# Kernel optimization log

Measured on AMD Instinct MI355X. Metric: run time of the kernel, lower is better.

The kernel has to match this reference:

```python
import jax, jax.numpy as jnp
import numpy as np

INPUT_DIM = 1024
LATENT_DIM = 100
NUM_EMBEDDINGS = 21
COMMITMENT_COST = 0.1
BATCH = 65536


def setup_inputs() -> dict:
    key = jax.random.key(0)
    k_x, k_we, k_be, k_cb, k_wd, k_bd = jax.random.split(key, 6)
    x = jax.random.normal(k_x, (BATCH, INPUT_DIM), dtype=jnp.float32)
    # nn.Linear default init ~ U(-1/sqrt(fan_in), 1/sqrt(fan_in)); approx with scaled uniform
    s_e = 1.0 / np.sqrt(INPUT_DIM)
    W_enc = jax.random.uniform(k_we, (LATENT_DIM, INPUT_DIM), jnp.float32, -s_e, s_e)
    b_enc = jax.random.uniform(k_be, (LATENT_DIM,), jnp.float32, -s_e, s_e)
    # codebook init ~ U(-1/num_embeddings, 1/num_embeddings)
    s_c = 1.0 / NUM_EMBEDDINGS
    codebook = jax.random.uniform(k_cb, (NUM_EMBEDDINGS, LATENT_DIM), jnp.float32, -s_c, s_c)
    s_d = 1.0 / np.sqrt(LATENT_DIM)
    W_dec = jax.random.uniform(k_wd, (INPUT_DIM, LATENT_DIM), jnp.float32, -s_d, s_d)
    b_dec = jax.random.uniform(k_bd, (INPUT_DIM,), jnp.float32, -s_d, s_d)
    return {"x": x, "W_enc": W_enc, "b_enc": b_enc, "codebook": codebook,
            "W_dec": W_dec, "b_dec": b_dec}


def reference(x, W_enc, b_enc, codebook, W_dec, b_dec):
    # Encoder: (B, D_in) -> (B, L)
    z_e = x @ W_enc.T + b_enc
    # Squared L2 distances to codebook: (B, K)
    distances = (jnp.sum(z_e ** 2, axis=-1, keepdims=True)
                 + jnp.sum(codebook ** 2, axis=1)[None, :]
                 - 2.0 * (z_e @ codebook.T))
    encoding_indices = jnp.argmin(distances, axis=-1, keepdims=True)  # (B, 1) int
    z_q = codebook[encoding_indices[:, 0]]  # (B, L)
    sg = jax.lax.stop_gradient
    vq_loss = (jnp.mean((sg(z_q) - z_e) ** 2)
               + COMMITMENT_COST * jnp.mean((sg(z_e) - z_q) ** 2))
    # Straight-through estimator
    z_q_st = z_e + sg(z_q - z_e)
    # Decoder: (B, L) -> (B, D_in)
    x_recon = z_q_st @ W_dec.T + b_dec
    return (x_recon, vq_loss, encoding_indices)
```

## Files before the change

kernel.cpp:

```cpp
#include <hip/hip_runtime.h>
#include <hip/hip_bf16.h>

#define BATCH   65536
#define D       1024
#define L       100
#define C       21
#define NPAD    112

typedef __bf16 bf16x8 __attribute__((ext_vector_type(8)));
typedef float  f32x4  __attribute__((ext_vector_type(4)));

static constexpr size_t OFF_P  = 8192;
static constexpr size_t OFF_U  = OFF_P + (size_t)BATCH * 4;
static constexpr size_t OFF_T  = OFF_U + (size_t)C * D * 4;
static constexpr size_t OFF_R  = OFF_T + 128;
static constexpr size_t OFF_WB = OFF_R + (size_t)C * D * 4;

__global__ __launch_bounds__(256) void k_setup(
    const float* __restrict__ W_enc, const float* __restrict__ b_enc,
    const float* __restrict__ cb,    const float* __restrict__ W_dec,
    const float* __restrict__ b_dec,
    float* __restrict__ u, float* __restrict__ t, float* __restrict__ R,
    __bf16* __restrict__ Wb)
{
    int id = blockIdx.x * 256 + threadIdx.x;
    if (id < C * D) {
        int c = id >> 10, k = id & 1023;
        float s = 0.f;
        for (int j = 0; j < L; j++) s += cb[c * L + j] * W_enc[j * D + k];
        u[id] = s;
    } else if (id < 2 * C * D) {
        int i2 = id - C * D;
        int c = i2 >> 10, k = i2 & 1023;
        float s = 0.f;
        for (int j = 0; j < L; j++) s += cb[c * L + j] * W_dec[k * L + j];
        R[i2] = s + b_dec[k];
    } else if (id < 2 * C * D + NPAD * D) {
        int i3 = id - 2 * C * D;
        int n = i3 >> 10, k = i3 & 1023;
        Wb[i3] = (n < L) ? (__bf16)W_enc[n * D + k] : (__bf16)0.f;
    } else if (id < 2 * C * D + NPAD * D + C) {
        int c = id - 2 * C * D - NPAD * D;
        float s = 0.f, b2 = 0.f;
        for (int j = 0; j < L; j++) {
            float cv = cb[c * L + j];
            s  += cv * cv;
            b2 += b_enc[j] * cv;
        }
        t[c] = s - 2.f * b2;
    }
}

__global__ __launch_bounds__(256) void k_main(
    const float* __restrict__ x, const float* __restrict__ u,
    const float* __restrict__ t, const float* __restrict__ R,
    const __bf16* __restrict__ Wb, const float* __restrict__ b_enc,
    float* __restrict__ outR, float* __restrict__ outIdx,
    double* __restrict__ bsums)
{
    __shared__ float part[4][64][22];
    __shared__ float pbest[64];
    __shared__ int   idxs[64];
    __shared__ float bpart[16];

    const int lane = threadIdx.x & 63;
    const int wave = __builtin_amdgcn_readfirstlane(threadIdx.x >> 6);
    const int row0 = blockIdx.x * 64;
    const int n15  = lane & 15;
    const int q    = lane >> 4;

    float sacc[C];
#pragma unroll
    for (int c = 0; c < C; c++) sacc[c] = 0.f;
    f32x4 zacc[7];
#pragma unroll
    for (int nt = 0; nt < 7; nt++) zacc[nt] = (f32x4){0.f, 0.f, 0.f, 0.f};

    const float* xs = x + (size_t)(row0 + lane) * D + wave * 16;
    const float* ub = u + wave * 16;
    const float* xm = x + (size_t)(row0 + wave * 16 + n15) * D + q * 8;

    for (int k0 = 0; k0 < D; k0 += 64) {
#pragma unroll
        for (int j2 = 0; j2 < 4; j2++) {
            float4 xv = *(const float4*)(xs + k0 + j2 * 4);
#pragma unroll
            for (int c = 0; c < C; c++) {
                const float* uc = ub + c * D + k0 + j2 * 4;
                sacc[c] += xv.x * uc[0] + xv.y * uc[1] + xv.z * uc[2] + xv.w * uc[3];
            }
        }
#pragma unroll
        for (int ks = 0; ks < 2; ks++) {
            float4 a0 = *(const float4*)(xm + k0 + ks * 32);
            float4 a1 = *(const float4*)(xm + k0 + ks * 32 + 4);
            bf16x8 af;
            af[0] = (__bf16)a0.x; af[1] = (__bf16)a0.y; af[2] = (__bf16)a0.z; af[3] = (__bf16)a0.w;
            af[4] = (__bf16)a1.x; af[5] = (__bf16)a1.y; af[6] = (__bf16)a1.z; af[7] = (__bf16)a1.w;
#pragma unroll
            for (int nt = 0; nt < 7; nt++) {
                bf16x8 bfr = *(const bf16x8*)(Wb + (size_t)(nt * 16 + n15) * D + k0 + ks * 32 + q * 8);
                zacc[nt] = __builtin_amdgcn_mfma_f32_16x16x32_bf16(af, bfr, zacc[nt], 0, 0, 0);
            }
        }
        __builtin_amdgcn_s_barrier();
    }

#pragma unroll
    for (int c = 0; c < C; c++) part[wave][lane][c] = sacc[c];
    __syncthreads();
    if (wave == 0) {
        float best = 3.0e38f;
        int   bi   = 0;
#pragma unroll
        for (int c = 0; c < C; c++) {
            float s = part[0][lane][c] + part[1][lane][c]
                    + part[2][lane][c] + part[3][lane][c];
            float score = t[c] - 2.0f * s;
            if (score < best) { best = score; bi = c; }
        }
        idxs[lane]         = bi;
        pbest[lane]        = best;
        outIdx[row0 + lane] = (float)bi;
    }
    __syncthreads();

    float rn[4] = {0.f, 0.f, 0.f, 0.f};
#pragma unroll
    for (int nt = 0; nt < 7; nt++) {
        int col = nt * 16 + n15;
        float bn = (col < L) ? b_enc[col] : 0.f;
#pragma unroll
        for (int r = 0; r < 4; r++) {
            float z = zacc[nt][r] + bn;
            rn[r] += z * z;
        }
    }
#pragma unroll
    for (int off = 1; off < 16; off <<= 1) {
#pragma unroll
        for (int r = 0; r < 4; r++) rn[r] += __shfl_xor(rn[r], off, 64);
    }
    if (n15 == 0) {
        float s4 = 0.f;
#pragma unroll
        for (int r = 0; r < 4; r++) s4 += rn[r] + pbest[wave * 16 + q * 4 + r];
        bpart[wave * 4 + q] = s4;
    }
    __syncthreads();
    if (threadIdx.x == 0) {
        double bs = 0.0;
        for (int i = 0; i < 16; i++) bs += (double)bpart[i];
        bsums[blockIdx.x] = bs;
    }

    for (int r = 0; r < 64; r++) {
        int id = idxs[r];
        const f32x4 v = ((const f32x4*)(R + (size_t)id * D))[threadIdx.x];
        __builtin_nontemporal_store(v, ((f32x4*)(outR + (size_t)(row0 + r) * D)) + threadIdx.x);
    }
}

__global__ __launch_bounds__(256) void k_final(
    const double* __restrict__ bsums, float* __restrict__ out_loss)
{
    __shared__ double wsum[4];
    int t = threadIdx.x;
    double s = bsums[t] + bsums[t + 256] + bsums[t + 512] + bsums[t + 768];
    for (int off = 32; off; off >>= 1) s += __shfl_down(s, off, 64);
    if ((t & 63) == 0) wsum[t >> 6] = s;
    __syncthreads();
    if (t == 0) {
        double tot = wsum[0] + wsum[1] + wsum[2] + wsum[3];
        out_loss[0] = (float)(1.1 * tot / ((double)BATCH * (double)L));
    }
}

extern "C" void kernel_launch(void* const* d_in, const int* in_sizes, int n_in,
                              void* d_out, int out_size, void* d_ws, size_t ws_size,
                              hipStream_t stream) {
    const float* x     = (const float*)d_in[0];
    const float* W_enc = (const float*)d_in[1];
    const float* b_enc = (const float*)d_in[2];
    const float* cb    = (const float*)d_in[3];
    const float* W_dec = (const float*)d_in[4];
    const float* b_dec = (const float*)d_in[5];

    char*   ws    = (char*)d_ws;
    double* bsums = (double*)ws;
    float*  u     = (float*)(ws + OFF_U);
    float*  t     = (float*)(ws + OFF_T);
    float*  R     = (float*)(ws + OFF_R);
    __bf16* Wb    = (__bf16*)(ws + OFF_WB);

    float* outR    = (float*)d_out;
    float* outLoss = outR + (size_t)BATCH * D;
    float* outIdx  = outLoss + 1;

    k_setup<<<617, 256, 0, stream>>>(W_enc, b_enc, cb, W_dec, b_dec, u, t, R, Wb);
    k_main <<<BATCH / 64, 256, 0, stream>>>(x, u, t, R, Wb, b_enc, outR, outIdx, bsums);
    k_final<<<1, 256, 0, stream>>>(bsums, outLoss);
}
```

Baseline: 564.4 us.

## Stage x tiles through double-buffered LDS with register prefetch in main kernel

Each 64-column chunk of x is now loaded once per block with coalesced row-contiguous loads, prefetched into registers one chunk ahead, and stored into a double-buffered shared-memory tile. The scalar distance path and the MFMA A-operand both read from that tile instead of each issuing strided global loads of the same x data. The partial-sum scratch reuses the tile's storage, and launch bounds now request four blocks per CU. The aim is to remove duplicated, poorly coalesced global reads of x and to hide load latency. The cost is about 35KB of LDS per block, extra barriers, and more register pressure from the prefetch buffers.

```diff
diff --git a/kernel.cpp b/kernel.cpp
--- a/kernel.cpp
+++ b/kernel.cpp
@@ -6,6 +6,7 @@
 #define L       100
 #define C       21
 #define NPAD    112
+#define RP      68
 
 typedef __bf16 bf16x8 __attribute__((ext_vector_type(8)));
 typedef float  f32x4  __attribute__((ext_vector_type(4)));
@@ -51,17 +52,19 @@
     }
 }
 
-__global__ __launch_bounds__(256) void k_main(
+__global__ __launch_bounds__(256, 4) void k_main(
     const float* __restrict__ x, const float* __restrict__ u,
     const float* __restrict__ t, const float* __restrict__ R,
     const __bf16* __restrict__ Wb, const float* __restrict__ b_enc,
     float* __restrict__ outR, float* __restrict__ outIdx,
     double* __restrict__ bsums)
 {
-    __shared__ float part[4][64][22];
+    __shared__ float xch[2][64][RP];
     __shared__ float pbest[64];
     __shared__ int   idxs[64];
     __shared__ float bpart[16];
+    float* partf = &xch[0][0][0];
+#define PART(w, l, c) partf[(((w) * 64 + (l)) * 22) + (c)]
 
     const int lane = threadIdx.x & 63;
     const int wave = __builtin_amdgcn_readfirstlane(threadIdx.x >> 6);
@@ -69,6 +72,10 @@
     const int n15  = lane & 15;
     const int q    = lane >> 4;
 
+    const int srow = wave * 16 + (lane >> 4);
+    const int sgr  = lane & 15;
+    const float* sbase = x + (size_t)(row0 + srow) * D + sgr * 4;
+
     float sacc[C];
 #pragma unroll
     for (int c = 0; c < C; c++) sacc[c] = 0.f;
@@ -76,51 +83,75 @@
 #pragma unroll
     for (int nt = 0; nt < 7; nt++) zacc[nt] = (f32x4){0.f, 0.f, 0.f, 0.f};
 
-    const float* xs = x + (size_t)(row0 + lane) * D + wave * 16;
     const float* ub = u + wave * 16;
-    const float* xm = x + (size_t)(row0 + wave * 16 + n15) * D + q * 8;
-
-    for (int k0 = 0; k0 < D; k0 += 64) {
+    const int mrow = wave * 16 + n15;
+
+    f32x4 stg[4];
+#pragma unroll
+    for (int j = 0; j < 4; j++) stg[j] = *(const f32x4*)(sbase + j * 4 * D);
+#pragma unroll
+    for (int j = 0; j < 4; j++) *(f32x4*)(&xch[0][srow + j * 4][sgr * 4]) = stg[j];
+    __syncthreads();
+
+    int cur = 0;
+    for (int ch = 0; ch < 16; ch++) {
+        const int k0 = ch * 64;
+        if (ch < 15) {
+#pragma unroll
+            for (int j = 0; j < 4; j++)
+                stg[j] = *(const f32x4*)(sbase + j * 4 * D + (ch + 1) * 64);
+        }
+
+        const float* xb = &xch[cur][lane][0];
 #pragma unroll
         for (int j2 = 0; j2 < 4; j2++) {
-            float4 xv = *(const float4*)(xs + k0 + j2 * 4);
+            f32x4 xv = *(const f32x4*)(xb + wave * 16 + j2 * 4);
 #pragma unroll
             for (int c = 0; c < C; c++) {
                 const float* uc = ub + c * D + k0 + j2 * 4;
-                sacc[c] += xv.x * uc[0] + xv.y * uc[1] + xv.z * uc[2] + xv.w * uc[3];
+                sacc[c] += xv[0] * uc[0] + xv[1] * uc[1] + xv[2] * uc[2] + xv[3] * uc[3];
             }
         }
+
+        const float* mb = &xch[cur][mrow][0];
 #pragma unroll
         for (int ks = 0; ks < 2; ks++) {
-            float4 a0 = *(const float4*)(xm + k0 + ks * 32);
-            float4 a1 = *(const float4*)(xm + k0 + ks * 32 + 4);
+            f32x4 a0 = *(const f32x4*)(mb + ks * 32 + q * 8);
+            f32x4 a1 = *(const f32x4*)(mb + ks * 32 + q * 8 + 4);
             bf16x8 af;
-            af[0] = (__bf16)a0.x; af[1] = (__bf16)a0.y; af[2] = (__bf16)a0.z; af[3] = (__bf16)a0.w;
-            af[4] = (__bf16)a1.x; af[5] = (__bf16)a1.y; af[6] = (__bf16)a1.z; af[7] = (__bf16)a1.w;
+            af[0] = (__bf16)a0[0]; af[1] = (__bf16)a0[1]; af[2] = (__bf16)a0[2]; af[3] = (__bf16)a0[3];
+            af[4] = (__bf16)a1[0]; af[5] = (__bf16)a1[1]; af[6] = (__bf16)a1[2]; af[7] = (__bf16)a1[3];
 #pragma unroll
             for (int nt = 0; nt < 7; nt++) {
                 bf16x8 bfr = *(const bf16x8*)(Wb + (size_t)(nt * 16 + n15) * D + k0 + ks * 32 + q * 8);
                 zacc[nt] = __builtin_amdgcn_mfma_f32_16x16x32_bf16(af, bfr, zacc[nt], 0, 0, 0);
             }
         }
-        __builtin_amdgcn_s_barrier();
-    }
-
-#pragma unroll
-    for (int c = 0; c < C; c++) part[wave][lane][c] = sacc[c];
+
+        if (ch < 15) {
+#pragma unroll
+            for (int j = 0; j < 4; j++)
+                *(f32x4*)(&xch[cur ^ 1][srow + j * 4][sgr * 4]) = stg[j];
+        }
+        __syncthreads();
+        cur ^= 1;
+    }
+
+#pragma unroll
+    for (int c = 0; c < C; c++) PART(wave, lane, c) = sacc[c];
     __syncthreads();
     if (wave == 0) {
         float best = 3.0e38f;
         int   bi   = 0;
 #pragma unroll
         for (int c = 0; c < C; c++) {
-            float s = part[0][lane][c] + part[1][lane][c]
-                    + part[2][lane][c] + part[3][lane][c];
+            float s = PART(0, lane, c) + PART(1, lane, c)
+                    + PART(2, lane, c) + PART(3, lane, c);
             float score = t[c] - 2.0f * s;
             if (score < best) { best = score; bi = c; }
         }
-        idxs[lane]         = bi;
-        pbest[lane]        = best;
+        idxs[lane]          = bi;
+        pbest[lane]         = best;
         outIdx[row0 + lane] = (float)bi;
     }
     __syncthreads();
@@ -159,6 +190,7 @@
         const f32x4 v = ((const f32x4*)(R + (size_t)id * D))[threadIdx.x];
         __builtin_nontemporal_store(v, ((f32x4*)(outR + (size_t)(row0 + r) * D)) + threadIdx.x);
     }
+#undef PART
 }
 
 __global__ __launch_bounds__(256) void k_final(
```

After: 597.3 us. +5.8%, slower.
